# Optimization experiments

Measured on AMD Instinct MI355X. Metric: run time of the kernel, lower is better.

The kernel has to match this reference:

```python
import jax, jax.numpy as jnp
import numpy as np

D_MODEL = 1024
N_HEADS = 16
HEAD_DIM = D_MODEL // N_HEADS
BATCH = 1
SEQLEN = 4096


def setup_inputs() -> dict:
    key = jax.random.key(0)
    k1, k2, k3 = jax.random.split(key, 3)
    x = jax.random.normal(k1, (BATCH, SEQLEN, D_MODEL), dtype=jnp.float32)
    # match typical Dense init scale so softmax isn't saturated
    Wqkv = jax.random.normal(k2, (D_MODEL, 3 * D_MODEL), dtype=jnp.float32) / np.sqrt(D_MODEL)
    Wout = jax.random.normal(k3, (D_MODEL, D_MODEL), dtype=jnp.float32) / np.sqrt(D_MODEL)
    return {"x": x, "Wqkv": Wqkv, "Wout": Wout}


def reference(x, Wqkv, Wout):
    b, l, d = x.shape
    qkv = x @ Wqkv  # [b, l, 3d]
    q, k, v = jnp.split(qkv, 3, axis=-1)
    # [b, l, d] -> [b, h, l, hd]
    def to_heads(t):
        return t.reshape(b, l, N_HEADS, HEAD_DIM).transpose(0, 2, 1, 3)
    q, k, v = to_heads(q), to_heads(k), to_heads(v)
    scale = 1.0 / np.sqrt(HEAD_DIM)
    attn = jnp.einsum('bhld,bhsd->bhls', q, k) * scale  # [b,h,l,l]
    causal_mask = jnp.tril(jnp.ones((l, l), dtype=bool))
    attn = jnp.where(causal_mask, attn, -jnp.inf)
    attn = jax.nn.softmax(attn, axis=-1)
    out = jnp.einsum('bhls,bhsd->bhld', attn, v)  # [b,h,l,hd]
    out = out.transpose(0, 2, 1, 3).reshape(b, l, d)
    return out @ Wout
```

## Files before the change

kernel.cpp:

```cpp
#include <hip/hip_runtime.h>

#define SEQ 4096
#define DM 1024
#define NH 16
#define HD 64

typedef __attribute__((ext_vector_type(8))) short short8;
typedef __attribute__((ext_vector_type(4))) short short4v;
typedef __attribute__((ext_vector_type(2))) short short2v;
typedef __attribute__((ext_vector_type(4))) float float4v;
typedef __attribute__((ext_vector_type(4))) int int4v;

__device__ __forceinline__ short f2bf(float f) {
    union { float f; unsigned u; } v; v.f = f;
    unsigned u = v.u;
    return (short)((u + 0x7fffu + ((u >> 16) & 1u)) >> 16);
}
__device__ __forceinline__ int cvtpk(float lo, float hi) {
    int r;
    asm("v_cvt_pk_bf16_f32 %0, %1, %2" : "=v"(r) : "v"(lo), "v"(hi));
    return r;
}

__device__ __forceinline__ void gload_lds16(const void* g, void* l) {
    __builtin_amdgcn_global_load_lds(
        (const __attribute__((address_space(1))) void*)g,
        (__attribute__((address_space(3))) void*)l, 16, 0, 0);
}

__global__ void cast_x(const float* __restrict__ in, short* __restrict__ out, int n4) {
    int i = blockIdx.x * blockDim.x + threadIdx.x;
    if (i < n4) {
        float4v x = ((const float4v*)in)[i];
        short4v o;
        o[0] = f2bf(x[0]); o[1] = f2bf(x[1]); o[2] = f2bf(x[2]); o[3] = f2bf(x[3]);
        ((short4v*)out)[i] = o;
    }
}

__global__ void transpose_cast(const float* __restrict__ in, short* __restrict__ out,
                               int H, int W, int scaled_rows, float scale) {
    __shared__ float tile[32][33];
    int bx = blockIdx.x * 32, by = blockIdx.y * 32;
    int tx = threadIdx.x, ty = threadIdx.y;
#pragma unroll
    for (int i = 0; i < 32; i += 8)
        tile[ty + i][tx] = in[(by + ty + i) * W + bx + tx];
    __syncthreads();
#pragma unroll
    for (int i = 0; i < 32; i += 8) {
        int orow = bx + ty + i;
        float sc = (orow < scaled_rows) ? scale : 1.0f;
        out[orow * H + by + tx] = f2bf(tile[tx][ty + i] * sc);
    }
}

__global__ void transpose_v(const short* __restrict__ qkv, short* __restrict__ vt) {
    __shared__ short tile[64][66];
    int h = blockIdx.z;
    int l0 = blockIdx.x * 64;
    int tx = threadIdx.x, ty = threadIdx.y;
#pragma unroll
    for (int i = 0; i < 8; i++) {
        int r = ty + i * 8;
        short2v v = *(const short2v*)&qkv[(l0 + r) * (3 * DM) + 2 * DM + h * HD + 2 * tx];
        tile[r][2 * tx] = v[0];
        tile[r][2 * tx + 1] = v[1];
    }
    __syncthreads();
#pragma unroll
    for (int i = 0; i < 8; i++) {
        int d = ty + i * 8;
        short2v v;
        v[0] = tile[2 * tx][d];
        v[1] = tile[2 * tx + 1][d];
        int s = l0 + 2 * tx;
        int soff = (s & ~31) | ((s & 12) << 1) | ((s & 16) >> 2) | (s & 3);
        *(short2v*)&vt[(h * HD + d) * SEQ + soff] = v;
    }
}

template <typename OutT>
__global__ __launch_bounds__(256) void gemm_bt(const short* __restrict__ A,
                                               const short* __restrict__ BT,
                                               OutT* __restrict__ C,
                                               int M, int N, int K) {
    __shared__ short As[128 * 32];
    __shared__ short Bs[128 * 32];
    int tid  = threadIdx.x;
    int m0   = blockIdx.y * 128;
    int n0   = blockIdx.x * 128;
    int w    = tid >> 6, lane = tid & 63;
    int wm   = w >> 1,  wn   = w & 1;
    int quad = lane >> 4, l15 = lane & 15;
    int srow = lane >> 2;
    int scol = (lane & 3) * 8;

    float4v acc[4][4];
#pragma unroll
    for (int mi = 0; mi < 4; mi++)
#pragma unroll
        for (int ni = 0; ni < 4; ni++)
            acc[mi][ni] = {0.f, 0.f, 0.f, 0.f};

    for (int k0 = 0; k0 < K; k0 += 32) {
        __syncthreads();
#pragma unroll
        for (int t = 0; t < 2; t++) {
            int chunk = w * 2 + t;
            int r = chunk * 16 + srow;
            gload_lds16(&A[(m0 + r) * K + k0 + scol], &As[chunk * 16 * 32]);
            gload_lds16(&BT[(n0 + r) * K + k0 + scol], &Bs[chunk * 16 * 32]);
        }
        __syncthreads();
        short8 a[4], b[4];
#pragma unroll
        for (int mi = 0; mi < 4; mi++)
            a[mi] = *(const short8*)&As[(wm * 64 + mi * 16 + l15) * 32 + quad * 8];
#pragma unroll
        for (int ni = 0; ni < 4; ni++)
            b[ni] = *(const short8*)&Bs[(wn * 64 + ni * 16 + l15) * 32 + quad * 8];
#pragma unroll
        for (int mi = 0; mi < 4; mi++)
#pragma unroll
            for (int ni = 0; ni < 4; ni++)
                acc[mi][ni] = __builtin_amdgcn_mfma_f32_16x16x32_bf16(a[mi], b[ni], acc[mi][ni], 0, 0, 0);
    }

#pragma unroll
    for (int mi = 0; mi < 4; mi++)
#pragma unroll
        for (int ni = 0; ni < 4; ni++)
#pragma unroll
            for (int r = 0; r < 4; r++) {
                int row = m0 + wm * 64 + mi * 16 + quad * 4 + r;
                int col = n0 + wn * 64 + ni * 16 + l15;
                float v = acc[mi][ni][r];
                if constexpr (sizeof(OutT) == 2) C[row * N + col] = (OutT)f2bf(v);
                else                             C[row * N + col] = (OutT)v;
            }
}

__global__ __launch_bounds__(256) void gemm_bt64(const short* __restrict__ A,
                                                 const short* __restrict__ BT,
                                                 float* __restrict__ C,
                                                 int M, int N, int K) {
    __shared__ short As[64 * 32];
    __shared__ short Bs[128 * 32];
    int tid  = threadIdx.x;
    int m0   = blockIdx.y * 64;
    int n0   = blockIdx.x * 128;
    int w    = tid >> 6, lane = tid & 63;
    int wm   = w >> 1,  wn   = w & 1;
    int quad = lane >> 4, l15 = lane & 15;
    int srow = lane >> 2;
    int scol = (lane & 3) * 8;

    float4v acc[2][4];
#pragma unroll
    for (int mi = 0; mi < 2; mi++)
#pragma unroll
        for (int ni = 0; ni < 4; ni++)
            acc[mi][ni] = {0.f, 0.f, 0.f, 0.f};

    for (int k0 = 0; k0 < K; k0 += 32) {
        __syncthreads();
        {
            int r = w * 16 + srow;
            gload_lds16(&A[(m0 + r) * K + k0 + scol], &As[w * 16 * 32]);
        }
#pragma unroll
        for (int t = 0; t < 2; t++) {
            int chunk = w * 2 + t;
            int r = chunk * 16 + srow;
            gload_lds16(&BT[(n0 + r) * K + k0 + scol], &Bs[chunk * 16 * 32]);
        }
        __syncthreads();
        short8 a[2], b[4];
#pragma unroll
        for (int mi = 0; mi < 2; mi++)
            a[mi] = *(const short8*)&As[(wm * 32 + mi * 16 + l15) * 32 + quad * 8];
#pragma unroll
        for (int ni = 0; ni < 4; ni++)
            b[ni] = *(const short8*)&Bs[(wn * 64 + ni * 16 + l15) * 32 + quad * 8];
#pragma unroll
        for (int mi = 0; mi < 2; mi++)
#pragma unroll
            for (int ni = 0; ni < 4; ni++)
                acc[mi][ni] = __builtin_amdgcn_mfma_f32_16x16x32_bf16(a[mi], b[ni], acc[mi][ni], 0, 0, 0);
    }

#pragma unroll
    for (int mi = 0; mi < 2; mi++)
#pragma unroll
        for (int ni = 0; ni < 4; ni++)
#pragma unroll
            for (int r = 0; r < 4; r++) {
                int row = m0 + wm * 32 + mi * 16 + quad * 4 + r;
                int col = n0 + wn * 64 + ni * 16 + l15;
                C[row * N + col] = acc[mi][ni][r];
            }
}

__global__ __launch_bounds__(256) void attn_kernel(const short* __restrict__ qkv,
                                                   const short* __restrict__ vtp,
                                                   float* __restrict__ Of0,
                                                   float* __restrict__ Of1,
                                                   float* __restrict__ Of2,
                                                   float* __restrict__ Lf0,
                                                   float* __restrict__ Lf1,
                                                   float* __restrict__ Lf2) {
    __shared__ short Ks[64 * 72];
    __shared__ short Vs[64 * 72];
    int gid = blockIdx.x;
    int rr = gid & 7, qq = gid >> 3;
    int hb = qq / 48;
    int rem = qq - hb * 48;
    int h = rr + 8 * hb;
    int b = rem & 15;
    int j = rem >> 4;
    float* __restrict__ Of = (j == 0) ? Of0 : (j == 1) ? Of1 : Of2;
    float* __restrict__ Lf = (j == 0) ? Lf0 : (j == 1) ? Lf1 : Lf2;
    int B0 = 2 * b + 2;

    int tid = threadIdx.x;
    int w = tid >> 6, lane = tid & 63;
    int quad = lane >> 4, l15 = lane & 15;
    int r8 = lane >> 3, c8 = lane & 7;
    int srow = w * 16 + r8;

    const short* Kg = qkv + DM + h * HD;
    const short* Vg = vtp + (h * HD) * SEQ;

    short8 onesv;
#pragma unroll
    for (int i = 0; i < 8; i++) onesv[i] = (short)0x3F80;

#pragma unroll 1
    for (int sg = 0; sg < 2; sg++) {
        int t, st0, stN;
        if (sg == 0) {
            t = b;
            st0 = 22 * j;
            stN = (22 * j + 22 < B0) ? 22 * j + 22 : B0;
        } else {
            t = 31 - b;
            int a0 = 22 * j - B0;
            st0 = (a0 > 0) ? a0 : 0;
            stN = 22 * j + 22 - B0;
        }
        if (st0 >= stN) continue;

        int q0 = t * 128;
        int qw = q0 + w * 32;

        short8 aq[2][2];
#pragma unroll
        for (int mi = 0; mi < 2; mi++)
#pragma unroll
            for (int kk = 0; kk < 2; kk++)
                aq[mi][kk] = *(const short8*)&qkv[(qw + mi * 16 + l15) * (3 * DM) + h * HD + kk * 32 + quad * 8];

        float4v lacc[2];
        float4v o[2][4];
#pragma unroll
        for (int mi = 0; mi < 2; mi++) {
            lacc[mi] = {0.f, 0.f, 0.f, 0.f};
#pragma unroll
            for (int dt = 0; dt < 4; dt++)
                o[mi][dt] = {0.f, 0.f, 0.f, 0.f};
        }

        short8 kg[2], vg[2];
        int sb = st0 * 64;
#pragma unroll
        for (int i = 0; i < 2; i++) {
            kg[i] = *(const short8*)&Kg[(sb + srow + 8 * i) * (3 * DM) + c8 * 8];
            vg[i] = *(const short8*)&Vg[(srow + 8 * i) * SEQ + sb + c8 * 8];
        }

        for (int tt = st0; tt < stN; tt++) {
            int s0 = tt * 64;
            int sn = (tt + 1 < stN) ? s0 + 64 : s0;

#pragma unroll
            for (int i = 0; i < 2; i++) {
                *(short8*)&Ks[(srow + 8 * i) * 72 + c8 * 8] = kg[i];
                *(short8*)&Vs[(srow + 8 * i) * 72 + c8 * 8] = vg[i];
            }
            asm volatile("s_waitcnt lgkmcnt(0)" ::: "memory");
            __builtin_amdgcn_s_barrier();
            __builtin_amdgcn_sched_barrier(0);

#pragma unroll
            for (int i = 0; i < 2; i++) {
                kg[i] = *(const short8*)&Kg[(sn + srow + 8 * i) * (3 * DM) + c8 * 8];
                vg[i] = *(const short8*)&Vg[(srow + 8 * i) * SEQ + sn + c8 * 8];
            }

            short8 kc[8], vc[8];
#pragma unroll
            for (int ni = 0; ni < 4; ni++)
#pragma unroll
                for (int kk = 0; kk < 2; kk++)
                    kc[ni * 2 + kk] = *(const short8*)&Ks[(ni * 16 + l15) * 72 + kk * 32 + quad * 8];
#pragma unroll
            for (int dt = 0; dt < 4; dt++)
#pragma unroll
                for (int pr = 0; pr < 2; pr++)
                    vc[dt * 2 + pr] = *(const short8*)&Vs[(dt * 16 + l15) * 72 + pr * 32 + quad * 8];

            float4v s[2][4];
#pragma unroll
            for (int mi = 0; mi < 2; mi++)
#pragma unroll
                for (int ni = 0; ni < 4; ni++) {
                    float4v a = {0.f, 0.f, 0.f, 0.f};
#pragma unroll
                    for (int kk = 0; kk < 2; kk++)
                        a = __builtin_amdgcn_mfma_f32_16x16x32_bf16(kc[ni * 2 + kk], aq[mi][kk], a, 0, 0, 0);
                    s[mi][ni] = a;
                }

            bool diag = (s0 + 63 > qw);
            short8 pa[2][2];
#pragma unroll
            for (int mi = 0; mi < 2; mi++) {
                int qrow = qw + mi * 16 + l15;
#pragma unroll
                for (int ni = 0; ni < 4; ni++) {
#pragma unroll
                    for (int r = 0; r < 4; r++) {
                        float p = __builtin_amdgcn_exp2f(s[mi][ni][r]);
                        if (diag) {
                            int scol = s0 + ni * 16 + quad * 4 + r;
                            p = (scol <= qrow) ? p : 0.f;
                        }
                        s[mi][ni][r] = p;
                    }
                }
#pragma unroll
                for (int pr = 0; pr < 2; pr++) {
                    int4v wpk;
                    wpk[0] = cvtpk(s[mi][2 * pr][0], s[mi][2 * pr][1]);
                    wpk[1] = cvtpk(s[mi][2 * pr][2], s[mi][2 * pr][3]);
                    wpk[2] = cvtpk(s[mi][2 * pr + 1][0], s[mi][2 * pr + 1][1]);
                    wpk[3] = cvtpk(s[mi][2 * pr + 1][2], s[mi][2 * pr + 1][3]);
                    pa[mi][pr] = *(short8*)&wpk;
                }
            }
#pragma unroll
            for (int mi = 0; mi < 2; mi++)
#pragma unroll
                for (int pr = 0; pr < 2; pr++)
                    lacc[mi] = __builtin_amdgcn_mfma_f32_16x16x32_bf16(pa[mi][pr], onesv, lacc[mi], 0, 0, 0);
#pragma unroll
            for (int mi = 0; mi < 2; mi++)
#pragma unroll
                for (int dt = 0; dt < 4; dt++)
#pragma unroll
                    for (int pr = 0; pr < 2; pr++)
                        o[mi][dt] = __builtin_amdgcn_mfma_f32_16x16x32_bf16(pa[mi][pr], vc[dt * 2 + pr], o[mi][dt], 0, 0, 0);

            asm volatile("s_waitcnt lgkmcnt(0)" ::: "memory");
            __builtin_amdgcn_s_barrier();
            __builtin_amdgcn_sched_barrier(0);
        }

#pragma unroll
        for (int mi = 0; mi < 2; mi++)
#pragma unroll
            for (int r = 0; r < 4; r++) {
                int row = qw + mi * 16 + quad * 4 + r;
#pragma unroll
                for (int dt = 0; dt < 4; dt++)
                    Of[row * DM + h * HD + dt * 16 + l15] = o[mi][dt][r];
            }
        if (l15 == 0) {
#pragma unroll
            for (int mi = 0; mi < 2; mi++)
#pragma unroll
                for (int r = 0; r < 4; r++)
                    Lf[h * SEQ + qw + mi * 16 + quad * 4 + r] = lacc[mi][r];
        }
    }
}

__global__ void attn_finalize(const float* __restrict__ Of0, const float* __restrict__ Of1,
                              const float* __restrict__ Of2,
                              const float* __restrict__ Lf0, const float* __restrict__ Lf1,
                              const float* __restrict__ Lf2,
                              short* __restrict__ ao) {
    int i = blockIdx.x * blockDim.x + threadIdx.x;
    int q  = i >> 8;
    int c4 = i & 255;
    int h  = c4 >> 4;
    int t  = q >> 7;
    bool lowq = (t < 16);
    int b = lowq ? t : 31 - t;
    bool use0 = lowq || (b <= 9);
    bool use1 = (!lowq) || (b >= 11);
    bool use2 = !lowq;

    float l = 0.f;
    float4v acc = {0.f, 0.f, 0.f, 0.f};
    if (use0) {
        l += Lf0[h * SEQ + q];
        float4v a = ((const float4v*)Of0)[i];
        acc[0] += a[0]; acc[1] += a[1]; acc[2] += a[2]; acc[3] += a[3];
    }
    if (use1) {
        l += Lf1[h * SEQ + q];
        float4v a = ((const float4v*)Of1)[i];
        acc[0] += a[0]; acc[1] += a[1]; acc[2] += a[2]; acc[3] += a[3];
    }
    if (use2) {
        l += Lf2[h * SEQ + q];
        float4v a = ((const float4v*)Of2)[i];
        acc[0] += a[0]; acc[1] += a[1]; acc[2] += a[2]; acc[3] += a[3];
    }
    float inv = 1.0f / l;
    short4v o;
    o[0] = f2bf(acc[0] * inv);
    o[1] = f2bf(acc[1] * inv);
    o[2] = f2bf(acc[2] * inv);
    o[3] = f2bf(acc[3] * inv);
    ((short4v*)ao)[i] = o;
}

extern "C" void kernel_launch(void* const* d_in, const int* in_sizes, int n_in,
                              void* d_out, int out_size, void* d_ws, size_t ws_size,
                              hipStream_t stream) {
    const float* x    = (const float*)d_in[0];
    const float* Wqkv = (const float*)d_in[1];
    const float* Wout = (const float*)d_in[2];
    float* out = (float*)d_out;

    char* ws = (char*)d_ws;
    short* xb    = (short*)(ws);
    short* wqkvT = (short*)(ws + 8388608);
    float* Of0   = (float*)(ws);
    float* Of1   = (float*)(d_out);
    short* qkv   = (short*)(ws + 16777216);
    short* vt    = (short*)(ws + 41943040);
    short* ao    = (short*)(ws + 50331648);
    float* Of2   = (float*)(ws + 58720256);
    float* Lf0   = (float*)(ws + 75497472);
    float* Lf1   = (float*)(ws + 75759616);
    float* Lf2   = (float*)(ws + 76021760);
    short* woutT = (short*)(ws + 76283904);

    const float SC = 0.18033688011112042f;

    cast_x<<<4096, 256, 0, stream>>>(x, xb, (SEQ * DM) / 4);
    transpose_cast<<<dim3(3 * DM / 32, DM / 32), dim3(32, 8), 0, stream>>>(Wqkv, wqkvT, DM, 3 * DM, DM, SC);
    transpose_cast<<<dim3(DM / 32, DM / 32), dim3(32, 8), 0, stream>>>(Wout, woutT, DM, DM, 0, 1.0f);

    gemm_bt<short><<<dim3(3 * DM / 128, SEQ / 128), 256, 0, stream>>>(xb, wqkvT, qkv, SEQ, 3 * DM, DM);

    transpose_v<<<dim3(SEQ / 64, 1, NH), dim3(32, 8), 0, stream>>>(qkv, vt);

    attn_kernel<<<768, 256, 0, stream>>>(qkv, vt, Of0, Of1, Of2, Lf0, Lf1, Lf2);
    attn_finalize<<<(SEQ * DM / 4) / 256, 256, 0, stream>>>(Of0, Of1, Of2, Lf0, Lf1, Lf2, ao);

    gemm_bt64<<<dim3(DM / 128, SEQ / 64), 256, 0, stream>>>(ao, woutT, out, SEQ, DM, DM);
}
```

Baseline: 209.9 us.

## Double-buffer K/V LDS tiles, add MFMA priority hints and split diagonal masking

Switches the attention kernel's K/V shared-memory tiles to double buffering. The next tile is written to the alternate buffer after the current tile's fragments are read, which drops one of the two barriers per iteration. It also wraps the MFMA blocks in s_setprio, hoists the causal-diagonal branch out of the exp loop, and sets launch bounds to 3 blocks per CU. The doubled LDS use and the extra register pressure may limit occupancy.

```diff
diff --git a/kernel.cpp b/kernel.cpp
--- a/kernel.cpp
+++ b/kernel.cpp
@@ -202,16 +202,16 @@
             }
 }
 
-__global__ __launch_bounds__(256) void attn_kernel(const short* __restrict__ qkv,
-                                                   const short* __restrict__ vtp,
-                                                   float* __restrict__ Of0,
-                                                   float* __restrict__ Of1,
-                                                   float* __restrict__ Of2,
-                                                   float* __restrict__ Lf0,
-                                                   float* __restrict__ Lf1,
-                                                   float* __restrict__ Lf2) {
-    __shared__ short Ks[64 * 72];
-    __shared__ short Vs[64 * 72];
+__global__ __launch_bounds__(256, 3) void attn_kernel(const short* __restrict__ qkv,
+                                                      const short* __restrict__ vtp,
+                                                      float* __restrict__ Of0,
+                                                      float* __restrict__ Of1,
+                                                      float* __restrict__ Of2,
+                                                      float* __restrict__ Lf0,
+                                                      float* __restrict__ Lf1,
+                                                      float* __restrict__ Lf2) {
+    __shared__ short Ks[2][64 * 72];
+    __shared__ short Vs[2][64 * 72];
     int gid = blockIdx.x;
     int rr = gid & 7, qq = gid >> 3;
     int hb = qq / 48;
@@ -272,45 +272,69 @@
         }
 
         short8 kg[2], vg[2];
-        int sb = st0 * 64;
-#pragma unroll
-        for (int i = 0; i < 2; i++) {
-            kg[i] = *(const short8*)&Kg[(sb + srow + 8 * i) * (3 * DM) + c8 * 8];
-            vg[i] = *(const short8*)&Vg[(srow + 8 * i) * SEQ + sb + c8 * 8];
-        }
-
-        for (int tt = st0; tt < stN; tt++) {
-            int s0 = tt * 64;
-            int sn = (tt + 1 < stN) ? s0 + 64 : s0;
-
+        {
+            int sb = st0 * 64;
 #pragma unroll
             for (int i = 0; i < 2; i++) {
-                *(short8*)&Ks[(srow + 8 * i) * 72 + c8 * 8] = kg[i];
-                *(short8*)&Vs[(srow + 8 * i) * 72 + c8 * 8] = vg[i];
+                kg[i] = *(const short8*)&Kg[(sb + srow + 8 * i) * (3 * DM) + c8 * 8];
+                vg[i] = *(const short8*)&Vg[(srow + 8 * i) * SEQ + sb + c8 * 8];
+            }
+#pragma unroll
+            for (int i = 0; i < 2; i++) {
+                *(short8*)&Ks[0][(srow + 8 * i) * 72 + c8 * 8] = kg[i];
+                *(short8*)&Vs[0][(srow + 8 * i) * 72 + c8 * 8] = vg[i];
+            }
+            if (st0 + 1 < stN) {
+                int s1 = (st0 + 1) * 64;
+#pragma unroll
+                for (int i = 0; i < 2; i++) {
+                    kg[i] = *(const short8*)&Kg[(s1 + srow + 8 * i) * (3 * DM) + c8 * 8];
+                    vg[i] = *(const short8*)&Vg[(srow + 8 * i) * SEQ + s1 + c8 * 8];
+                }
             }
             asm volatile("s_waitcnt lgkmcnt(0)" ::: "memory");
             __builtin_amdgcn_s_barrier();
             __builtin_amdgcn_sched_barrier(0);
-
-#pragma unroll
-            for (int i = 0; i < 2; i++) {
-                kg[i] = *(const short8*)&Kg[(sn + srow + 8 * i) * (3 * DM) + c8 * 8];
-                vg[i] = *(const short8*)&Vg[(srow + 8 * i) * SEQ + sn + c8 * 8];
-            }
+        }
+
+        int cur = 0;
+        for (int tt = st0; tt < stN; tt++) {
+            int s0 = tt * 64;
+            const short* Kb = &Ks[cur][0];
+            const short* Vb = &Vs[cur][0];
+            short* Kn = &Ks[cur ^ 1][0];
+            short* Vn = &Vs[cur ^ 1][0];
 
             short8 kc[8], vc[8];
 #pragma unroll
             for (int ni = 0; ni < 4; ni++)
 #pragma unroll
                 for (int kk = 0; kk < 2; kk++)
-                    kc[ni * 2 + kk] = *(const short8*)&Ks[(ni * 16 + l15) * 72 + kk * 32 + quad * 8];
+                    kc[ni * 2 + kk] = *(const short8*)&Kb[(ni * 16 + l15) * 72 + kk * 32 + quad * 8];
 #pragma unroll
             for (int dt = 0; dt < 4; dt++)
 #pragma unroll
                 for (int pr = 0; pr < 2; pr++)
-                    vc[dt * 2 + pr] = *(const short8*)&Vs[(dt * 16 + l15) * 72 + pr * 32 + quad * 8];
+                    vc[dt * 2 + pr] = *(const short8*)&Vb[(dt * 16 + l15) * 72 + pr * 32 + quad * 8];
+
+            if (tt + 1 < stN) {
+#pragma unroll
+                for (int i = 0; i < 2; i++) {
+                    *(short8*)&Kn[(srow + 8 * i) * 72 + c8 * 8] = kg[i];
+                    *(short8*)&Vn[(srow + 8 * i) * 72 + c8 * 8] = vg[i];
+                }
+                if (tt + 2 < stN) {
+                    int s2 = (tt + 2) * 64;
+#pragma unroll
+                    for (int i = 0; i < 2; i++) {
+                        kg[i] = *(const short8*)&Kg[(s2 + srow + 8 * i) * (3 * DM) + c8 * 8];
+                        vg[i] = *(const short8*)&Vg[(srow + 8 * i) * SEQ + s2 + c8 * 8];
+                    }
+                }
+            }
 
             float4v s[2][4];
+            __builtin_amdgcn_s_setprio(1);
 #pragma unroll
             for (int mi = 0; mi < 2; mi++)
 #pragma unroll
@@ -321,24 +345,34 @@
                         a = __builtin_amdgcn_mfma_f32_16x16x32_bf16(kc[ni * 2 + kk], aq[mi][kk], a, 0, 0, 0);
                     s[mi][ni] = a;
                 }
+            __builtin_amdgcn_s_setprio(0);
 
             bool diag = (s0 + 63 > qw);
+            if (diag) {
+#pragma unroll
+                for (int mi = 0; mi < 2; mi++) {
+                    int qrow = qw + mi * 16 + l15;
+#pragma unroll
+                    for (int ni = 0; ni < 4; ni++)
+#pragma unroll
+                        for (int r = 0; r < 4; r++) {
+                            float p = __builtin_amdgcn_exp2f(s[mi][ni][r]);
+                            int scol = s0 + ni * 16 + quad * 4 + r;
+                            s[mi][ni][r] = (scol <= qrow) ? p : 0.f;
+                        }
+                }
+            } else {
+#pragma unroll
+                for (int mi = 0; mi < 2; mi++)
+#pragma unroll
+                    for (int ni = 0; ni < 4; ni++)
+#pragma unroll
+                        for (int r = 0; r < 4; r++)
+                            s[mi][ni][r] = __builtin_amdgcn_exp2f(s[mi][ni][r]);
+            }
             short8 pa[2][2];
 #pragma unroll
-            for (int mi = 0; mi < 2; mi++) {
-                int qrow = qw + mi * 16 + l15;
-#pragma unroll
-                for (int ni = 0; ni < 4; ni++) {
-#pragma unroll
-                    for (int r = 0; r < 4; r++) {
-                        float p = __builtin_amdgcn_exp2f(s[mi][ni][r]);
-                        if (diag) {
-                            int scol = s0 + ni * 16 + quad * 4 + r;
-                            p = (scol <= qrow) ? p : 0.f;
-                        }
-                        s[mi][ni][r] = p;
-                    }
-                }
+            for (int mi = 0; mi < 2; mi++)
 #pragma unroll
                 for (int pr = 0; pr < 2; pr++) {
                     int4v wpk;
@@ -348,7 +382,8 @@
                     wpk[3] = cvtpk(s[mi][2 * pr + 1][2], s[mi][2 * pr + 1][3]);
                     pa[mi][pr] = *(short8*)&wpk;
                 }
-            }
+
+            __builtin_amdgcn_s_setprio(1);
 #pragma unroll
             for (int mi = 0; mi < 2; mi++)
 #pragma unroll
@@ -361,10 +396,12 @@
 #pragma unroll
                     for (int pr = 0; pr < 2; pr++)
                         o[mi][dt] = __builtin_amdgcn_mfma_f32_16x16x32_bf16(pa[mi][pr], vc[dt * 2 + pr], o[mi][dt], 0, 0, 0);
+            __builtin_amdgcn_s_setprio(0);
 
             asm volatile("s_waitcnt lgkmcnt(0)" ::: "memory");
             __builtin_amdgcn_s_barrier();
             __builtin_amdgcn_sched_barrier(0);
+            cur ^= 1;
         }
 
 #pragma unroll
```

After: 241.9 us. 1.15x slower.

## Double-buffer K/V tiles via direct global-to-LDS loads with XOR swizzle

Applied to the files above, without the earlier changes.

The attention kernel now stages K and V tiles straight into double-buffered LDS using global-to-LDS loads, instead of going through registers and then writing LDS. This removes one of the two barriers per iteration. The tiles use an unpadded 64-wide layout with an XOR swizzle to avoid bank conflicts. It also raises MFMA priority with s_setprio, splits masked and unmasked exp paths, and adds a launch-bounds occupancy hint of 2. In exchange it doubles LDS use and waits on vmcnt(0) at the end of each iteration, which can expose global load latency.

```diff
diff --git a/kernel.cpp b/kernel.cpp
--- a/kernel.cpp
+++ b/kernel.cpp
@@ -202,16 +202,16 @@
             }
 }
 
-__global__ __launch_bounds__(256) void attn_kernel(const short* __restrict__ qkv,
-                                                   const short* __restrict__ vtp,
-                                                   float* __restrict__ Of0,
-                                                   float* __restrict__ Of1,
-                                                   float* __restrict__ Of2,
-                                                   float* __restrict__ Lf0,
-                                                   float* __restrict__ Lf1,
-                                                   float* __restrict__ Lf2) {
-    __shared__ short Ks[64 * 72];
-    __shared__ short Vs[64 * 72];
+__global__ __launch_bounds__(256, 2) void attn_kernel(const short* __restrict__ qkv,
+                                                      const short* __restrict__ vtp,
+                                                      float* __restrict__ Of0,
+                                                      float* __restrict__ Of1,
+                                                      float* __restrict__ Of2,
+                                                      float* __restrict__ Lf0,
+                                                      float* __restrict__ Lf1,
+                                                      float* __restrict__ Lf2) {
+    __shared__ short Ks[2][64 * 64];
+    __shared__ short Vs[2][64 * 64];
     int gid = blockIdx.x;
     int rr = gid & 7, qq = gid >> 3;
     int hb = qq / 48;
@@ -226,8 +226,10 @@
     int tid = threadIdx.x;
     int w = tid >> 6, lane = tid & 63;
     int quad = lane >> 4, l15 = lane & 15;
-    int r8 = lane >> 3, c8 = lane & 7;
-    int srow = w * 16 + r8;
+    int rowb = w * 16;
+    int lrow = lane >> 3;
+    int cg   = (lane & 7) ^ lrow;
+    int xr   = (l15 & 7) * 8;
 
     const short* Kg = qkv + DM + h * HD;
     const short* Vg = vtp + (h * HD) * SEQ;
@@ -271,46 +273,42 @@
                 o[mi][dt] = {0.f, 0.f, 0.f, 0.f};
         }
 
-        short8 kg[2], vg[2];
-        int sb = st0 * 64;
-#pragma unroll
-        for (int i = 0; i < 2; i++) {
-            kg[i] = *(const short8*)&Kg[(sb + srow + 8 * i) * (3 * DM) + c8 * 8];
-            vg[i] = *(const short8*)&Vg[(srow + 8 * i) * SEQ + sb + c8 * 8];
-        }
-
+        auto stage = [&](int buf, int s0) {
+#pragma unroll
+            for (int i = 0; i < 2; i++) {
+                int r = rowb + i * 8;
+                gload_lds16(&Kg[(s0 + r + lrow) * (3 * DM) + cg * 8], &Ks[buf][r * 64]);
+                gload_lds16(&Vg[(r + lrow) * SEQ + s0 + cg * 8],      &Vs[buf][r * 64]);
+            }
+        };
+
+        stage(0, st0 * 64);
+        asm volatile("s_waitcnt vmcnt(0)" ::: "memory");
+        __builtin_amdgcn_s_barrier();
+        __builtin_amdgcn_sched_barrier(0);
+
+        int cur = 0;
         for (int tt = st0; tt < stN; tt++) {
             int s0 = tt * 64;
-            int sn = (tt + 1 < stN) ? s0 + 64 : s0;
-
-#pragma unroll
-            for (int i = 0; i < 2; i++) {
-                *(short8*)&Ks[(srow + 8 * i) * 72 + c8 * 8] = kg[i];
-                *(short8*)&Vs[(srow + 8 * i) * 72 + c8 * 8] = vg[i];
-            }
-            asm volatile("s_waitcnt lgkmcnt(0)" ::: "memory");
-            __builtin_amdgcn_s_barrier();
-            __builtin_amdgcn_sched_barrier(0);
-
-#pragma unroll
-            for (int i = 0; i < 2; i++) {
-                kg[i] = *(const short8*)&Kg[(sn + srow + 8 * i) * (3 * DM) + c8 * 8];
-                vg[i] = *(const short8*)&Vg[(srow + 8 * i) * SEQ + sn + c8 * 8];
-            }
+            if (tt + 1 < stN) stage(cur ^ 1, s0 + 64);
+
+            const short* Kb = &Ks[cur][0];
+            const short* Vb = &Vs[cur][0];
 
             short8 kc[8], vc[8];
 #pragma unroll
             for (int ni = 0; ni < 4; ni++)
 #pragma unroll
                 for (int kk = 0; kk < 2; kk++)
-                    kc[ni * 2 + kk] = *(const short8*)&Ks[(ni * 16 + l15) * 72 + kk * 32 + quad * 8];
+                    kc[ni * 2 + kk] = *(const short8*)&Kb[(ni * 16 + l15) * 64 + (((kk * 4 + quad) * 8) ^ xr)];
 #pragma unroll
             for (int dt = 0; dt < 4; dt++)
 #pragma unroll
                 for (int pr = 0; pr < 2; pr++)
-                    vc[dt * 2 + pr] = *(const short8*)&Vs[(dt * 16 + l15) * 72 + pr * 32 + quad * 8];
+                    vc[dt * 2 + pr] = *(const short8*)&Vb[(dt * 16 + l15) * 64 + (((pr * 4 + quad) * 8) ^ xr)];
 
             float4v s[2][4];
+            __builtin_amdgcn_s_setprio(1);
 #pragma unroll
             for (int mi = 0; mi < 2; mi++)
 #pragma unroll
@@ -321,24 +319,34 @@
                         a = __builtin_amdgcn_mfma_f32_16x16x32_bf16(kc[ni * 2 + kk], aq[mi][kk], a, 0, 0, 0);
                     s[mi][ni] = a;
                 }
+            __builtin_amdgcn_s_setprio(0);
 
             bool diag = (s0 + 63 > qw);
+            if (diag) {
+#pragma unroll
+                for (int mi = 0; mi < 2; mi++) {
+                    int qrow = qw + mi * 16 + l15;
+#pragma unroll
+                    for (int ni = 0; ni < 4; ni++)
+#pragma unroll
+                        for (int r = 0; r < 4; r++) {
+                            float p = __builtin_amdgcn_exp2f(s[mi][ni][r]);
+                            int scol = s0 + ni * 16 + quad * 4 + r;
+                            s[mi][ni][r] = (scol <= qrow) ? p : 0.f;
+                        }
+                }
+            } else {
+#pragma unroll
+                for (int mi = 0; mi < 2; mi++)
+#pragma unroll
+                    for (int ni = 0; ni < 4; ni++)
+#pragma unroll
+                        for (int r = 0; r < 4; r++)
+                            s[mi][ni][r] = __builtin_amdgcn_exp2f(s[mi][ni][r]);
+            }
             short8 pa[2][2];
 #pragma unroll
-            for (int mi = 0; mi < 2; mi++) {
-                int qrow = qw + mi * 16 + l15;
-#pragma unroll
-                for (int ni = 0; ni < 4; ni++) {
-#pragma unroll
-                    for (int r = 0; r < 4; r++) {
-                        float p = __builtin_amdgcn_exp2f(s[mi][ni][r]);
-                        if (diag) {
-                            int scol = s0 + ni * 16 + quad * 4 + r;
-                            p = (scol <= qrow) ? p : 0.f;
-                        }
-                        s[mi][ni][r] = p;
-                    }
-                }
+            for (int mi = 0; mi < 2; mi++)
 #pragma unroll
                 for (int pr = 0; pr < 2; pr++) {
                     int4v wpk;
@@ -348,7 +356,8 @@
                     wpk[3] = cvtpk(s[mi][2 * pr + 1][2], s[mi][2 * pr + 1][3]);
                     pa[mi][pr] = *(short8*)&wpk;
                 }
-            }
+
+            __builtin_amdgcn_s_setprio(1);
 #pragma unroll
             for (int mi = 0; mi < 2; mi++)
 #pragma unroll
@@ -361,10 +370,12 @@
 #pragma unroll
                     for (int pr = 0; pr < 2; pr++)
                         o[mi][dt] = __builtin_amdgcn_mfma_f32_16x16x32_bf16(pa[mi][pr], vc[dt * 2 + pr], o[mi][dt], 0, 0, 0);
-
-            asm volatile("s_waitcnt lgkmcnt(0)" ::: "memory");
+            __builtin_amdgcn_s_setprio(0);
+
+            asm volatile("s_waitcnt vmcnt(0) lgkmcnt(0)" ::: "memory");
             __builtin_amdgcn_s_barrier();
             __builtin_amdgcn_sched_barrier(0);
+            cur ^= 1;
         }
 
 #pragma unroll
```

Measured after the change: 204.9 us. 1.02x faster.
